# Performance work log

Measured on AMD Instinct MI355X. Metric: run time of the kernel, lower is better.

The kernel has to match this reference:

```python
import jax, jax.numpy as jnp
import numpy as np

HEADS = 16
LN_EPS = 1e-6

def _layernorm(x, scale, bias):
    mu = jnp.mean(x, axis=-1, keepdims=True)
    var = jnp.mean(jnp.square(x - mu), axis=-1, keepdims=True)
    return (x - mu) * jax.lax.rsqrt(var + LN_EPS) * scale + bias

def setup_inputs() -> dict:
    key = jax.random.key(0)
    ks = jax.random.split(key, 5)
    B, L, D, F = 2, 2048, 1024, 4096
    s = lambda fan_in: 1.0 / np.sqrt(fan_in)
    return {
        'x': jax.random.normal(ks[0], (B, L, D), jnp.float32),
        'ln1_scale': jnp.ones((D,), jnp.float32),
        'ln1_bias': jnp.zeros((D,), jnp.float32),
        'w_qkv': jax.random.normal(ks[1], (D, 3 * D), jnp.float32) * s(D),
        'w_proj': jax.random.normal(ks[2], (D, D), jnp.float32) * s(D),
        'b_proj': jnp.zeros((D,), jnp.float32),
        'ln2_scale': jnp.ones((D,), jnp.float32),
        'ln2_bias': jnp.zeros((D,), jnp.float32),
        'w_mlp1': jax.random.normal(ks[3], (D, F), jnp.float32) * s(D),
        'b_mlp1': jnp.zeros((F,), jnp.float32),
        'w_mlp2': jax.random.normal(ks[4], (F, D), jnp.float32) * s(F),
        'b_mlp2': jnp.zeros((D,), jnp.float32),
    }

def reference(x, ln1_scale, ln1_bias, w_qkv, w_proj, b_proj,
              ln2_scale, ln2_bias, w_mlp1, b_mlp1, w_mlp2, b_mlp2):
    B, L, D = x.shape
    H = HEADS
    hd = D // H
    # pre-norm attention
    h = _layernorm(x, ln1_scale, ln1_bias)
    qkv = h @ w_qkv  # [B,L,3D]
    q, k, v = jnp.split(qkv, 3, axis=-1)
    q = q.reshape(B, L, H, hd).transpose(0, 2, 1, 3)  # [B,H,L,hd]
    k = k.reshape(B, L, H, hd).transpose(0, 2, 1, 3)
    v = v.reshape(B, L, H, hd).transpose(0, 2, 1, 3)
    scale = jnp.sqrt(jnp.float32(hd))
    scores = jnp.einsum('bhqd,bhkd->bhqk', q, k) / scale  # [B,H,L,L]
    attn = jax.nn.softmax(scores, axis=-1)
    out = jnp.einsum('bhqk,bhkd->bhqd', attn, v)  # [B,H,L,hd]
    out = out.transpose(0, 2, 1, 3).reshape(B, L, D)
    x = x + out @ w_proj + b_proj
    # pre-norm MLP
    h = _layernorm(x, ln2_scale, ln2_bias)
    m = jax.nn.gelu(h @ w_mlp1 + b_mlp1, approximate=True)
    return x + m @ w_mlp2 + b_mlp2
```

## Files before the change

kernel.cpp:

```cpp
#include <hip/hip_runtime.h>
#include <hip/hip_bf16.h>
#include <cstdint>
#include <cstddef>

typedef __bf16 bf16;
typedef __bf16 bf16x8 __attribute__((ext_vector_type(8)));
typedef float f32x4 __attribute__((ext_vector_type(4)));
typedef short short4v __attribute__((ext_vector_type(4)));
typedef unsigned uint2v __attribute__((ext_vector_type(2)));

#define GLB_AS(p) ((const __attribute__((address_space(1))) unsigned*)(unsigned long long)(p))
#define LDS_AS(p) ((__attribute__((address_space(3))) unsigned*)(unsigned)(unsigned long long)(p))

__device__ __forceinline__ void g2l16(const void* g, void* l) {
  __builtin_amdgcn_global_load_lds(GLB_AS(g), LDS_AS(l), 16, 0, 0);
}

__device__ __forceinline__ short f2bf(float x) {
  bf16 h = (bf16)x;
  return __builtin_bit_cast(short, h);
}

__device__ __forceinline__ unsigned pk_bf16(float a, float b) {
  __hip_bfloat162 h = __float22bfloat162_rn(float2{a, b});
  unsigned u;
  __builtin_memcpy(&u, &h, 4);
  return u;
}

extern "C" __device__ __attribute__((const)) float __ocml_native_exp2_f32(float);
extern "C" __device__ __attribute__((const)) float __ocml_native_recip_f32(float);
__device__ __forceinline__ float fast_exp2(float x) {
  return __ocml_native_exp2_f32(x);
}
__device__ __forceinline__ float fast_tanh(float a) {
  float e = __ocml_native_exp2_f32(a * 2.8853900817779268f);
  return 1.f - 2.f * __ocml_native_recip_f32(e + 1.f);
}

constexpr int MROWS = 4096;
constexpr size_t ATILE = (size_t)MROWS * 32;

#define QSCALE 0.18033688011112042f

__device__ __forceinline__ void transpose_body(
    const float* __restrict__ in, bf16* __restrict__ out, int K, int N,
    int bx, int by, float (*tile)[33], int tid)
{
  int tx = tid & 31, ty = tid >> 5;
  int n0 = bx * 32, k0 = by * 32;
  for (int i = ty; i < 32; i += 8)
    tile[i][tx] = in[(size_t)(k0 + i) * N + n0 + tx];
  __syncthreads();
  bf16* obase = out + (size_t)(k0 >> 5) * N * 32;
  for (int i = ty; i < 32; i += 8)
    obase[(size_t)(n0 + i) * 32 + tx] = (bf16)tile[tx][i];
}

__device__ __forceinline__ void ln_body(
    const float* __restrict__ x, const float* __restrict__ sc,
    const float* __restrict__ bi, bf16* __restrict__ out,
    int row, float* wsum, float* wsq, int tid)
{
  const float* xr = x + (size_t)row * 1024;
  int c = tid * 4;
  float4 xv = *(const float4*)(xr + c);
  float s = xv.x + xv.y + xv.z + xv.w;
  float q = xv.x * xv.x + xv.y * xv.y + xv.z * xv.z + xv.w * xv.w;
#pragma unroll
  for (int off = 1; off < 64; off <<= 1) {
    s += __shfl_xor(s, off);
    q += __shfl_xor(q, off);
  }
  int wv = tid >> 6;
  if ((tid & 63) == 0) { wsum[wv] = s; wsq[wv] = q; }
  __syncthreads();
  s = wsum[0] + wsum[1] + wsum[2] + wsum[3];
  q = wsq[0] + wsq[1] + wsq[2] + wsq[3];
  float mean = s * (1.f / 1024.f);
  float var = q * (1.f / 1024.f) - mean * mean;
  float rstd = rsqrtf(var + 1e-6f);
  float4 scv = *(const float4*)(sc + c);
  float4 biv = *(const float4*)(bi + c);
  bf16* o = out + (size_t)(c >> 5) * ATILE + (size_t)row * 32 + (c & 31);
  o[0] = (bf16)((xv.x - mean) * rstd * scv.x + biv.x);
  o[1] = (bf16)((xv.y - mean) * rstd * scv.y + biv.y);
  o[2] = (bf16)((xv.z - mean) * rstd * scv.z + biv.z);
  o[3] = (bf16)((xv.w - mean) * rstd * scv.w + biv.w);
}

__global__ __launch_bounds__(256) void prep_kernel(
    const float* __restrict__ wqkv, const float* __restrict__ wproj,
    const float* __restrict__ wmlp1, const float* __restrict__ wmlp2,
    bf16* __restrict__ wqkv_t, bf16* __restrict__ wproj_t,
    bf16* __restrict__ wmlp1_t, bf16* __restrict__ wmlp2_t,
    const float* __restrict__ x, const float* __restrict__ ln1s,
    const float* __restrict__ ln1b, bf16* __restrict__ hbuf)
{
  __shared__ float tile[32][33];
  __shared__ float wsum[4], wsq[4];
  int bid = blockIdx.x, tid = threadIdx.x;
  if (bid < 3072)
    transpose_body(wqkv, wqkv_t, 1024, 3072, bid % 96, bid / 96, tile, tid);
  else if (bid < 4096) {
    int i = bid - 3072;
    transpose_body(wproj, wproj_t, 1024, 1024, i % 32, i / 32, tile, tid);
  } else if (bid < 8192) {
    int i = bid - 4096;
    transpose_body(wmlp1, wmlp1_t, 1024, 4096, i % 128, i / 128, tile, tid);
  } else if (bid < 12288) {
    int i = bid - 8192;
    transpose_body(wmlp2, wmlp2_t, 4096, 1024, i % 32, i / 32, tile, tid);
  } else {
    ln_body(x, ln1s, ln1b, hbuf, bid - 12288, wsum, wsq, tid);
  }
}

__global__ __launch_bounds__(256) void ln_kernel(
    const float* __restrict__ x, const float* __restrict__ sc,
    const float* __restrict__ bi, bf16* __restrict__ out)
{
  __shared__ float wsum[4], wsq[4];
  ln_body(x, sc, bi, out, blockIdx.x, wsum, wsq, threadIdx.x);
}

template <int MT, int NT, int KS, int EPI>
__global__ __launch_bounds__(256) void gemm_tt(
    const bf16* __restrict__ A, const bf16* __restrict__ Bt,
    int N, int K,
    const float* __restrict__ bias, const float* __restrict__ resid,
    float* __restrict__ outf, bf16* __restrict__ ob0,
    bf16* __restrict__ ob1, bf16* __restrict__ ob2)
{
  constexpr int TM = MT * 32, TN = NT * 32;
  __shared__ __align__(16) bf16 As[2][TM * 32 * KS];
  __shared__ __align__(16) bf16 Bs[2][TN * 32 * KS];
  const int tid = threadIdx.x, lane = tid & 63, wave = tid >> 6;
  const int wm = wave >> 1, wn = wave & 1;
  const int quad = lane >> 4, l16 = lane & 15;

  int flat = blockIdx.x + gridDim.x * blockIdx.y;
  int xcd = flat & 7, rr = flat >> 3;
  int npx = gridDim.x >> 3;
  int bn = xcd * npx + (rr % npx);
  int bm = rr / npx;

  const size_t astride = ATILE;
  const size_t bstride = (size_t)N * 32;
  const bf16* Abase = A + (size_t)bm * TM * 32 + (size_t)lane * 8;
  const bf16* Bbase = Bt + (size_t)bn * TN * 32 + (size_t)lane * 8;

  f32x4 acc[MT][NT] = {};
  const int KT = K / (32 * KS);

  auto stage = [&](int buf, int kt) {
#pragma unroll
    for (int ks = 0; ks < KS; ks++) {
      const bf16* Ab = Abase + (size_t)(kt * KS + ks) * astride;
      const bf16* Bb = Bbase + (size_t)(kt * KS + ks) * bstride;
#pragma unroll
      for (int i = 0; i < MT / 2; i++)
        g2l16(Ab + (wave + 4 * i) * 512, &As[buf][ks * TM * 32 + (wave + 4 * i) * 512]);
#pragma unroll
      for (int i = 0; i < NT / 2; i++)
        g2l16(Bb + (wave + 4 * i) * 512, &Bs[buf][ks * TN * 32 + (wave + 4 * i) * 512]);
    }
  };

  stage(0, 0);
  int buf = 0;
  for (int kt = 0; kt < KT; kt++) {
    __syncthreads();
    if (kt + 1 < KT) stage(buf ^ 1, kt + 1);
#pragma unroll
    for (int kk = 0; kk < KS; kk++) {
      bf16x8 af[MT], bfr[NT];
#pragma unroll
      for (int mt = 0; mt < MT; mt++)
        af[mt] = *(const bf16x8*)&As[buf][kk * TM * 32 + (wm * MT * 16 + mt * 16 + l16) * 32 + quad * 8];
#pragma unroll
      for (int nt = 0; nt < NT; nt++)
        bfr[nt] = *(const bf16x8*)&Bs[buf][kk * TN * 32 + (wn * NT * 16 + nt * 16 + l16) * 32 + quad * 8];
#pragma unroll
      for (int mt = 0; mt < MT; mt++)
#pragma unroll
        for (int nt = 0; nt < NT; nt++)
          acc[mt][nt] = __builtin_amdgcn_mfma_f32_16x16x32_bf16(af[mt], bfr[nt], acc[mt][nt], 0, 0, 0);
    }
    buf ^= 1;
  }

#pragma unroll
  for (int mt = 0; mt < MT; mt++) {
#pragma unroll
    for (int nt = 0; nt < NT; nt++) {
      int row0 = bm * TM + wm * MT * 16 + mt * 16 + quad * 4;
      int col = bn * TN + wn * NT * 16 + nt * 16 + l16;
      if (EPI == 0) {
        int b = row0 >> 11, l = row0 & 2047;
        int which = col >> 10, d = col & 1023;
        int hh = d >> 6, hdi = d & 63;
        size_t bh = (size_t)(b * 16 + hh);
        if (which == 0) {
#pragma unroll
          for (int r = 0; r < 4; r++)
            ob0[(bh * 2048 + l + r) * 64 + hdi] = (bf16)(acc[mt][nt][r] * QSCALE);
        } else if (which == 1) {
#pragma unroll
          for (int r = 0; r < 4; r++)
            ob1[(bh * 2048 + l + r) * 64 + hdi] = (bf16)acc[mt][nt][r];
        } else {
          short4v v4;
#pragma unroll
          for (int r = 0; r < 4; r++) v4[r] = f2bf(acc[mt][nt][r]);
          *(short4v*)&ob2[(bh * 64 + hdi) * 2048 + l] = v4;
        }
      } else {
#pragma unroll
        for (int r = 0; r < 4; r++) {
          int row = row0 + r;
          float v = acc[mt][nt][r];
          if (EPI == 1) {
            size_t idx = (size_t)row * N + col;
            outf[idx] = v + bias[col] + resid[idx];
          } else {
            float t = v + bias[col];
            float a = 0.7978845608028654f * t * (1.f + 0.044715f * t * t);
            float g = 0.5f * t * (1.f + fast_tanh(a));
            ob0[(size_t)(col >> 5) * ATILE + (size_t)row * 32 + (col & 31)] = (bf16)g;
          }
        }
      }
    }
  }
}

__global__ __launch_bounds__(512, 2) void gemm8p_gelu(
    const bf16* __restrict__ A, const bf16* __restrict__ Bt,
    const float* __restrict__ bias, bf16* __restrict__ ob0)
{
  __shared__ __align__(16) bf16 As[4 * 8192];
  __shared__ __align__(16) bf16 Bs[4 * 8192];
  const int tid = threadIdx.x, lane = tid & 63, wave = tid >> 6;
  const int quad = lane >> 4, l16 = lane & 15;
  const int wm = wave >> 2, wn = wave & 3;

  int flat = blockIdx.x + gridDim.x * blockIdx.y;
  int xcd = flat & 7, rr = flat >> 3;
  int bn = xcd * 2 + (rr & 1);
  int bm = rr >> 1;

  auto stA = [&](int buf, int ktile, int half) {
    const bf16* g = A + (size_t)ktile * ATILE +
                    ((size_t)bm * 256 + half * 128) * 32 + (size_t)tid * 8;
    g2l16(g, &As[(buf * 2 + (ktile & 1)) * 8192 + half * 4096 + wave * 512]);
  };
  auto stB = [&](int buf, int ktile, int half) {
    const bf16* g = Bt + (size_t)ktile * ATILE +
                    ((size_t)bn * 256 + half * 128) * 32 + (size_t)tid * 8;
    g2l16(g, &Bs[(buf * 2 + (ktile & 1)) * 8192 + half * 4096 + wave * 512]);
  };

  f32x4 acc[8][4] = {};
  bf16x8 af[4][2], bfr[4][2];

  stA(0, 0, 0); stA(0, 0, 1); stA(0, 1, 0); stA(0, 1, 1);
  stB(0, 0, 0); stB(0, 0, 1); stB(0, 1, 0); stB(0, 1, 1);
  asm volatile("s_waitcnt vmcnt(0)" ::: "memory");
  __builtin_amdgcn_s_barrier();

  for (int kt = 0; kt < 16; kt++) {
    const int buf = kt & 1, nbuf = buf ^ 1;
    const bool more = (kt + 1) < 16;
    const int kA = (kt + 1) * 2;

#pragma unroll
    for (int mt = 0; mt < 4; mt++)
#pragma unroll
      for (int kk = 0; kk < 2; kk++)
        af[mt][kk] = *(const bf16x8*)&As[(buf * 2 + kk) * 8192 +
                       (wm * 128 + mt * 16 + l16) * 32 + quad * 8];
#pragma unroll
    for (int nt = 0; nt < 2; nt++)
#pragma unroll
      for (int kk = 0; kk < 2; kk++)
        bfr[nt][kk] = *(const bf16x8*)&Bs[(buf * 2 + kk) * 8192 +
                        (wn * 64 + nt * 16 + l16) * 32 + quad * 8];
    if (more) { stA(nbuf, kA, 0); stA(nbuf, kA, 1); stA(nbuf, kA + 1, 0); stA(nbuf, kA + 1, 1); }
    __builtin_amdgcn_s_barrier();
    asm volatile("s_waitcnt lgkmcnt(0)" ::: "memory");
    __builtin_amdgcn_sched_barrier(0);
    __builtin_amdgcn_s_setprio(1);
#pragma unroll
    for (int mt = 0; mt < 4; mt++)
#pragma unroll
      for (int nt = 0; nt < 2; nt++)
#pragma unroll
        for (int kk = 0; kk < 2; kk++)
          acc[mt][nt] = __builtin_amdgcn_mfma_f32_16x16x32_bf16(af[mt][kk], bfr[nt][kk], acc[mt][nt], 0, 0, 0);
    __builtin_amdgcn_s_setprio(0);
    __builtin_amdgcn_s_barrier();

#pragma unroll
    for (int nt = 2; nt < 4; nt++)
#pragma unroll
      for (int kk = 0; kk < 2; kk++)
        bfr[nt][kk] = *(const bf16x8*)&Bs[(buf * 2 + kk) * 8192 +
                        (wn * 64 + nt * 16 + l16) * 32 + quad * 8];
    if (more) { stB(nbuf, kA, 0); stB(nbuf, kA, 1); stB(nbuf, kA + 1, 0); stB(nbuf, kA + 1, 1); }
    __builtin_amdgcn_s_barrier();
    asm volatile("s_waitcnt lgkmcnt(0)" ::: "memory");
    __builtin_amdgcn_sched_barrier(0);
    __builtin_amdgcn_s_setprio(1);
#pragma unroll
    for (int mt = 0; mt < 4; mt++)
#pragma unroll
      for (int nt = 2; nt < 4; nt++)
#pragma unroll
        for (int kk = 0; kk < 2; kk++)
          acc[mt][nt] = __builtin_amdgcn_mfma_f32_16x16x32_bf16(af[mt][kk], bfr[nt][kk], acc[mt][nt], 0, 0, 0);
    __builtin_amdgcn_s_setprio(0);
    __builtin_amdgcn_s_barrier();

#pragma unroll
    for (int mt = 0; mt < 4; mt++)
#pragma unroll
      for (int kk = 0; kk < 2; kk++)
        af[mt][kk] = *(const bf16x8*)&As[(buf * 2 + kk) * 8192 +
                       (wm * 128 + (mt + 4) * 16 + l16) * 32 + quad * 8];
    __builtin_amdgcn_s_barrier();
    asm volatile("s_waitcnt lgkmcnt(0)" ::: "memory");
    __builtin_amdgcn_sched_barrier(0);
    __builtin_amdgcn_s_setprio(1);
#pragma unroll
    for (int mt = 0; mt < 4; mt++)
#pragma unroll
      for (int nt = 0; nt < 2; nt++)
#pragma unroll
        for (int kk = 0; kk < 2; kk++)
          acc[mt + 4][nt] = __builtin_amdgcn_mfma_f32_16x16x32_bf16(af[mt][kk], bfr[nt][kk], acc[mt + 4][nt], 0, 0, 0);
    __builtin_amdgcn_s_setprio(0);
    __builtin_amdgcn_s_barrier();

    __builtin_amdgcn_s_setprio(1);
#pragma unroll
    for (int mt = 0; mt < 4; mt++)
#pragma unroll
      for (int nt = 2; nt < 4; nt++)
#pragma unroll
        for (int kk = 0; kk < 2; kk++)
          acc[mt + 4][nt] = __builtin_amdgcn_mfma_f32_16x16x32_bf16(af[mt][kk], bfr[nt][kk], acc[mt + 4][nt], 0, 0, 0);
    __builtin_amdgcn_s_setprio(0);
    asm volatile("s_waitcnt vmcnt(0)" ::: "memory");
    __builtin_amdgcn_s_barrier();
  }

#pragma unroll
  for (int mt = 0; mt < 8; mt++) {
#pragma unroll
    for (int nt = 0; nt < 4; nt++) {
      int row0 = bm * 256 + wm * 128 + mt * 16 + quad * 4;
      int col = bn * 256 + wn * 64 + nt * 16 + l16;
      float bcol = bias[col];
#pragma unroll
      for (int r = 0; r < 4; r++) {
        int row = row0 + r;
        float t = acc[mt][nt][r] + bcol;
        float a = 0.7978845608028654f * t * (1.f + 0.044715f * t * t);
        float g = 0.5f * t * (1.f + fast_tanh(a));
        ob0[(size_t)(col >> 5) * ATILE + (size_t)row * 32 + (col & 31)] = (bf16)g;
      }
    }
  }
}

__global__ __launch_bounds__(256, 2) void flash_attn(
    const bf16* __restrict__ Q, const bf16* __restrict__ Kg,
    const bf16* __restrict__ Vg, bf16* __restrict__ O)
{
  __shared__ __align__(16) bf16 Ks[128 * 64];
  __shared__ __align__(16) bf16 Vs[64 * 128];
  const int tid = threadIdx.x, lane = tid & 63, wave = tid >> 6;
  const int quad = lane >> 4, l16 = lane & 15;
  const int qt = blockIdx.x, bh = blockIdx.y;
  const int b = bh >> 4, h = bh & 15;

  const bf16* qg = Q + ((size_t)bh * 2048 + qt * 128) * 64;
  const bf16* kg = Kg + (size_t)bh * 2048 * 64;
  const bf16* vg = Vg + (size_t)bh * 64 * 2048;

  const int kw0 = ((tid >> 3) << 7) + (((tid & 7) << 4) ^ (((tid >> 3) & 7) << 4));
  const int vw0 = ((tid >> 4) << 8) + (((tid & 15) << 4) ^ (((tid >> 4) & 7) << 4));

  bf16x8 qf[2][2];
#pragma unroll
  for (int s = 0; s < 2; s++)
#pragma unroll
    for (int kk = 0; kk < 2; kk++)
      qf[s][kk] = *(const bf16x8*)&qg[(size_t)(wave * 32 + s * 16 + l16) * 64 + kk * 32 + quad * 8];

  f32x4 oacc[2][4] = {};
  float lrow[2] = {0.f, 0.f};

  bf16x8 kreg[4], vreg[4];
#pragma unroll
  for (int i = 0; i < 4; i++) {
    int t = tid + i * 256;
    kreg[i] = *(const bf16x8*)&kg[(size_t)(t >> 3) * 64 + (t & 7) * 8];
    vreg[i] = *(const bf16x8*)&vg[(size_t)(t >> 4) * 2048 + (t & 15) * 8];
  }

  for (int kt = 0; kt < 16; kt++) {
    __syncthreads();
#pragma unroll
    for (int i = 0; i < 4; i++) {
      *(bf16x8*)((char*)Ks + kw0 + i * 4096) = kreg[i];
      *(bf16x8*)((char*)Vs + vw0 + i * 4096) = vreg[i];
    }
    __syncthreads();
    if (kt < 15) {
#pragma unroll
      for (int i = 0; i < 4; i++) {
        int t = tid + i * 256;
        kreg[i] = *(const bf16x8*)&kg[((size_t)(kt + 1) * 128 + (t >> 3)) * 64 + (t & 7) * 8];
        vreg[i] = *(const bf16x8*)&vg[(size_t)(t >> 4) * 2048 + (kt + 1) * 128 + (t & 15) * 8];
      }
    }

    f32x4 sacc[2][8] = {};
#pragma unroll
    for (int kk = 0; kk < 2; kk++) {
#pragma unroll
      for (int ct = 0; ct < 8; ct++) {
        int krow = ct * 16 + l16;
        bf16x8 kf = *(const bf16x8*)((const char*)Ks + krow * 128 +
                                     ((kk * 64 + quad * 16) ^ ((l16 & 7) << 4)));
        sacc[0][ct] = __builtin_amdgcn_mfma_f32_16x16x32_bf16(kf, qf[0][kk], sacc[0][ct], 0, 0, 0);
        sacc[1][ct] = __builtin_amdgcn_mfma_f32_16x16x32_bf16(kf, qf[1][kk], sacc[1][ct], 0, 0, 0);
      }
    }

    short4v pf[2][8];
#pragma unroll
    for (int s = 0; s < 2; s++) {
      float sum = 0.f;
#pragma unroll
      for (int ct = 0; ct < 8; ct++) {
        float p0 = fast_exp2(sacc[s][ct][0]);
        float p1 = fast_exp2(sacc[s][ct][1]);
        float p2 = fast_exp2(sacc[s][ct][2]);
        float p3 = fast_exp2(sacc[s][ct][3]);
        sum += (p0 + p1) + (p2 + p3);
        uint2v u;
        u[0] = pk_bf16(p0, p1);
        u[1] = pk_bf16(p2, p3);
        pf[s][ct] = __builtin_bit_cast(short4v, u);
      }
      lrow[s] += sum;
    }

#pragma unroll
    for (int ot = 0; ot < 4; ot++) {
#pragma unroll
      for (int ct = 0; ct < 8; ct++) {
        int vrow = ot * 16 + l16;
        short4v vf = *(const short4v*)((const char*)Vs + vrow * 256 +
                                       ((ct * 32 + quad * 8) ^ ((l16 & 7) << 4)));
        oacc[0][ot] = __builtin_amdgcn_mfma_f32_16x16x16bf16_1k(vf, pf[0][ct], oacc[0][ot], 0, 0, 0);
        oacc[1][ot] = __builtin_amdgcn_mfma_f32_16x16x16bf16_1k(vf, pf[1][ct], oacc[1][ot], 0, 0, 0);
      }
    }
  }

#pragma unroll
  for (int s = 0; s < 2; s++) {
    float l = lrow[s];
    l += __shfl_xor(l, 16);
    l += __shfl_xor(l, 32);
    float inv = 1.f / l;
    int qrow = qt * 128 + wave * 32 + s * 16 + l16;
    size_t grow = (size_t)b * 2048 + qrow;
#pragma unroll
    for (int ot = 0; ot < 4; ot++) {
      int col = h * 64 + ot * 16 + quad * 4;
      short4v o4;
#pragma unroll
      for (int r = 0; r < 4; r++) o4[r] = f2bf(oacc[s][ot][r] * inv);
      *(short4v*)&O[(size_t)(col >> 5) * ATILE + grow * 32 + (col & 31)] = o4;
    }
  }
}

extern "C" void kernel_launch(void* const* d_in, const int* in_sizes, int n_in,
                              void* d_out, int out_size, void* d_ws, size_t ws_size,
                              hipStream_t stream)
{
  const float* x     = (const float*)d_in[0];
  const float* ln1s  = (const float*)d_in[1];
  const float* ln1b  = (const float*)d_in[2];
  const float* wqkv  = (const float*)d_in[3];
  const float* wproj = (const float*)d_in[4];
  const float* bproj = (const float*)d_in[5];
  const float* ln2s  = (const float*)d_in[6];
  const float* ln2b  = (const float*)d_in[7];
  const float* wmlp1 = (const float*)d_in[8];
  const float* bmlp1 = (const float*)d_in[9];
  const float* wmlp2 = (const float*)d_in[10];
  const float* bmlp2 = (const float*)d_in[11];
  float* out = (float*)d_out;

  char* ws = (char*)d_ws;
  bf16* wqkv_t  = (bf16*)(ws + 0);
  bf16* wproj_t = (bf16*)(ws + 6291456);
  bf16* wmlp1_t = (bf16*)(ws + 8388608);
  bf16* wmlp2_t = (bf16*)(ws + 16777216);
  bf16* hbuf    = (bf16*)(ws + 25165824);
  bf16* qb      = (bf16*)(ws + 33554432);
  bf16* kb      = (bf16*)(ws + 41943040);
  bf16* vb      = (bf16*)(ws + 50331648);
  bf16* aout    = (bf16*)(ws + 58720256);
  bf16* mbuf    = (bf16*)(ws + 33554432);

  prep_kernel<<<16384, 256, 0, stream>>>(wqkv, wproj, wmlp1, wmlp2,
                                         wqkv_t, wproj_t, wmlp1_t, wmlp2_t,
                                         x, ln1s, ln1b, hbuf);
  gemm_tt<4, 4, 1, 0><<<dim3(24, 32), 256, 0, stream>>>(hbuf, wqkv_t, 3072, 1024,
                                                        nullptr, nullptr, nullptr, qb, kb, vb);
  flash_attn<<<dim3(16, 32), 256, 0, stream>>>(qb, kb, vb, aout);
  gemm_tt<2, 4, 2, 1><<<dim3(8, 64), 256, 0, stream>>>(aout, wproj_t, 1024, 1024,
                                                       bproj, x, out, nullptr, nullptr, nullptr);
  ln_kernel<<<4096, 256, 0, stream>>>(out, ln2s, ln2b, hbuf);
  gemm8p_gelu<<<dim3(16, 16), 512, 0, stream>>>(hbuf, wmlp1_t, bmlp1, mbuf);
  gemm_tt<2, 4, 2, 1><<<dim3(8, 64), 256, 0, stream>>>(mbuf, wmlp2_t, 1024, 4096,
                                                       bmlp2, out, out, nullptr, nullptr, nullptr);
}
```

Before: 317.8 us.

## Use 16x16x32 bf16 MFMA for PV product with permuted K row layout

Switches the P·V product in flash attention from 16x16x16 MFMA to 16x16x32 MFMA, packing two score tiles into one 8-wide bf16 operand. K rows are permuted when written to LDS so the score accumulator layout lines up with the wider MFMA's k-dimension. V fragments are read as 16-byte loads. This halves the number of PV MFMA instructions and LDS reads, at the cost of a more intricate K-row permutation that must stay consistent with the V layout.

```diff
diff --git a/kernel.cpp b/kernel.cpp
--- a/kernel.cpp
+++ b/kernel.cpp
@@ -8,6 +8,7 @@
 typedef float f32x4 __attribute__((ext_vector_type(4)));
 typedef short short4v __attribute__((ext_vector_type(4)));
 typedef unsigned uint2v __attribute__((ext_vector_type(2)));
+typedef unsigned uint4v __attribute__((ext_vector_type(4)));
 
 #define GLB_AS(p) ((const __attribute__((address_space(1))) unsigned*)(unsigned long long)(p))
 #define LDS_AS(p) ((__attribute__((address_space(3))) unsigned*)(unsigned)(unsigned long long)(p))
@@ -389,7 +390,11 @@
   const bf16* kg = Kg + (size_t)bh * 2048 * 64;
   const bf16* vg = Vg + (size_t)bh * 64 * 2048;
 
-  const int kw0 = ((tid >> 3) << 7) + (((tid & 7) << 4) ^ (((tid >> 3) & 7) << 4));
+  const int a0 = tid >> 3;
+  const int a5 = a0 & 31;
+  const int vb = ((a5 >> 2) & 1) * 16 + (a5 >> 3) * 4 + (a5 & 3);
+  const int v0 = (a0 & ~31) + vb;
+  const int kw0 = (v0 << 7) + (((tid & 7) << 4) ^ ((v0 & 7) << 4));
   const int vw0 = ((tid >> 4) << 8) + (((tid & 15) << 4) ^ (((tid >> 4) & 7) << 4));
 
   bf16x8 qf[2][2];
@@ -440,21 +445,24 @@
       }
     }
 
-    short4v pf[2][8];
+    bf16x8 pf[2][4];
 #pragma unroll
     for (int s = 0; s < 2; s++) {
       float sum = 0.f;
 #pragma unroll
-      for (int ct = 0; ct < 8; ct++) {
-        float p0 = fast_exp2(sacc[s][ct][0]);
-        float p1 = fast_exp2(sacc[s][ct][1]);
-        float p2 = fast_exp2(sacc[s][ct][2]);
-        float p3 = fast_exp2(sacc[s][ct][3]);
-        sum += (p0 + p1) + (p2 + p3);
-        uint2v u;
-        u[0] = pk_bf16(p0, p1);
-        u[1] = pk_bf16(p2, p3);
-        pf[s][ct] = __builtin_bit_cast(short4v, u);
+      for (int c = 0; c < 4; c++) {
+        uint4v u;
+#pragma unroll
+        for (int bb = 0; bb < 2; bb++) {
+          float p0 = fast_exp2(sacc[s][2 * c + bb][0]);
+          float p1 = fast_exp2(sacc[s][2 * c + bb][1]);
+          float p2 = fast_exp2(sacc[s][2 * c + bb][2]);
+          float p3 = fast_exp2(sacc[s][2 * c + bb][3]);
+          sum += (p0 + p1) + (p2 + p3);
+          u[bb * 2 + 0] = pk_bf16(p0, p1);
+          u[bb * 2 + 1] = pk_bf16(p2, p3);
+        }
+        pf[s][c] = __builtin_bit_cast(bf16x8, u);
       }
       lrow[s] += sum;
     }
@@ -462,12 +470,12 @@
 #pragma unroll
     for (int ot = 0; ot < 4; ot++) {
 #pragma unroll
-      for (int ct = 0; ct < 8; ct++) {
+      for (int c = 0; c < 4; c++) {
         int vrow = ot * 16 + l16;
-        short4v vf = *(const short4v*)((const char*)Vs + vrow * 256 +
-                                       ((ct * 32 + quad * 8) ^ ((l16 & 7) << 4)));
-        oacc[0][ot] = __builtin_amdgcn_mfma_f32_16x16x16bf16_1k(vf, pf[0][ct], oacc[0][ot], 0, 0, 0);
-        oacc[1][ot] = __builtin_amdgcn_mfma_f32_16x16x16bf16_1k(vf, pf[1][ct], oacc[1][ot], 0, 0, 0);
+        bf16x8 vf = *(const bf16x8*)((const char*)Vs + vrow * 256 +
+                                     ((c * 64 + quad * 16) ^ ((l16 & 7) << 4)));
+        oacc[0][ot] = __builtin_amdgcn_mfma_f32_16x16x32_bf16(vf, pf[0][c], oacc[0][ot], 0, 0, 0);
+        oacc[1][ot] = __builtin_amdgcn_mfma_f32_16x16x32_bf16(vf, pf[1][c], oacc[1][ot], 0, 0, 0);
       }
     }
   }
```

New measurement: 310.3 us. 1.02x faster.
